# Performance work log

Hardware: AMD Instinct MI355X
Metric: run time of the kernel (lower is better)

The kernel has to match this reference:

```python
import jax, jax.numpy as jnp
import numpy as np

N_NODES = 100000
N_EDGES = 640000
D = 128
L = 3
NUM_GRAPHS = 128


def setup_inputs() -> dict:
    key = jax.random.key(0)
    ks = jax.random.split(key, 8)
    scale = 1.0 / np.sqrt(D)
    x = jax.random.normal(ks[0], (N_NODES, D), dtype=jnp.float32)
    edge_index = jax.random.randint(ks[1], (2, N_EDGES), 0, N_NODES, dtype=jnp.int64)
    batch = jnp.sort(jax.random.randint(ks[2], (N_NODES,), 0, NUM_GRAPHS, dtype=jnp.int64))
    W1 = jax.random.normal(ks[3], (L, D, D), dtype=jnp.float32) * scale
    b1 = jnp.zeros((L, D), dtype=jnp.float32)
    W2 = jax.random.normal(ks[4], (L, D, D), dtype=jnp.float32) * scale
    b2 = jnp.zeros((L, D), dtype=jnp.float32)
    return {"x": x, "edge_index": edge_index, "batch": batch,
            "W1": W1, "b1": b1, "W2": W2, "b2": b2}


def reference(x, edge_index, batch, W1, b1, W2, b2):
    # GIN forward: per layer z = ReLU(MLP((1+eps)*z + sum_{j in N(i)} z_j)), eps=0
    n = x.shape[0]
    src, dst = edge_index[0], edge_index[1]  # messages flow src -> dst
    z = x
    for l in range(W1.shape[0]):
        agg = jax.ops.segment_sum(z[src], dst, num_segments=n)  # scatter-add aggregation
        h = agg + z                                             # (1+eps)*x_i + sum x_j, eps=0
        h = jnp.maximum(h @ W1[l] + b1[l], 0.0)                 # Linear + ReLU
        z = h @ W2[l] + b2[l]                                   # Linear
        z = jnp.maximum(z, 0.0)                                 # F.relu after conv
    # global mean pool over graph ids (dropout is identity in eval / p=0)
    ones = jnp.ones((n,), dtype=z.dtype)
    counts = jax.ops.segment_sum(ones, batch, num_segments=NUM_GRAPHS)
    sums = jax.ops.segment_sum(z, batch, num_segments=NUM_GRAPHS)
    g = sums / jnp.maximum(counts, 1.0)[:, None]
    return z, g
```

## Files before the change

### kernel.cpp

```cpp
#include <hip/hip_runtime.h>
#include <hip/hip_bf16.h>

#define D 128
#define NG 128
#define PROWS 128

typedef __attribute__((ext_vector_type(8))) short bf16x8;
typedef __attribute__((ext_vector_type(4))) float f32x4;

__device__ inline unsigned short f2bf(float f) {
  union { float f; unsigned u; } c; c.f = f;
  unsigned u = c.u;
  return (unsigned short)((u + 0x7FFFu + ((u >> 16) & 1u)) >> 16);
}
__device__ inline float bf2f(unsigned short b) {
  union { unsigned u; float f; } c; c.u = ((unsigned)b) << 16;
  return c.f;
}

__global__ void prep_w(const float* __restrict__ W1, const float* __restrict__ W2,
                       unsigned short* __restrict__ Wt1, unsigned short* __restrict__ Wt2,
                       int* __restrict__ deg, int N) {
  int t = blockIdx.x * 256 + threadIdx.x;
  if (t < N) deg[t] = 0;
  if (t >= 3 * 128 * 128) return;
  int l = t >> 14, k = (t >> 7) & 127, n = t & 127;
  int o = (l << 14) + (n << 7) + k;
  Wt1[o] = f2bf(W1[t]);
  Wt2[o] = f2bf(W2[t]);
}


__global__ void hist_deg(const int* __restrict__ dst, int* __restrict__ deg, int E) {
  int e = blockIdx.x * 256 + threadIdx.x;
  if (e < E) atomicAdd(deg + dst[e], 1);
}

__global__ __launch_bounds__(256) void scan1(const int* __restrict__ deg,
    int* __restrict__ rowptr, int* __restrict__ bsum, int n) {
  __shared__ int sh[256];
  int tid = threadIdx.x;
  int idx = blockIdx.x * 1024 + tid * 4;
  int v[4], tsum = 0;
#pragma unroll
  for (int j = 0; j < 4; ++j) { v[j] = (idx + j < n) ? deg[idx + j] : 0; tsum += v[j]; }
  sh[tid] = tsum;
  __syncthreads();
  for (int off = 1; off < 256; off <<= 1) {
    int x = (tid >= off) ? sh[tid - off] : 0;
    __syncthreads();
    sh[tid] += x;
    __syncthreads();
  }
  if (tid == 255) bsum[blockIdx.x] = sh[255];
  int run = sh[tid] - tsum;
#pragma unroll
  for (int j = 0; j < 4; ++j) { if (idx + j < n) rowptr[idx + j] = run; run += v[j]; }
}

__global__ __launch_bounds__(128) void scan2(int* __restrict__ bsum, int nb) {
  __shared__ int sh[128];
  int tid = threadIdx.x;
  int v = (tid < nb) ? bsum[tid] : 0;
  sh[tid] = v;
  __syncthreads();
  for (int off = 1; off < 128; off <<= 1) {
    int x = (tid >= off) ? sh[tid - off] : 0;
    __syncthreads();
    sh[tid] += x;
    __syncthreads();
  }
  if (tid < nb) bsum[tid] = sh[tid] - v;
}

__global__ void scan3(int* __restrict__ rowptr, int* __restrict__ pos,
                      const int* __restrict__ bsum, int n, int E) {
  int t = blockIdx.x * 256 + threadIdx.x;
  if (t < n) {
    int v = rowptr[t] + bsum[t >> 10];
    rowptr[t] = v;
    pos[t] = v;
  }
  if (t == 0) rowptr[n] = E;
}

__global__ void edge_scatter(const int* __restrict__ src, const int* __restrict__ dst,
                             int* __restrict__ pos, int* __restrict__ csr_src, int E) {
  int e = blockIdx.x * 256 + threadIdx.x;
  if (e >= E) return;
  int idx = atomicAdd(pos + dst[e], 1);
  csr_src[idx] = src[e];
}


template<bool IN_BF16, bool LAST>
__global__ __launch_bounds__(256) void layer_fused(const void* __restrict__ zin,
    const int* __restrict__ rowptr, const int* __restrict__ csr_src,
    const unsigned short* __restrict__ Wt1, const float* __restrict__ b1v,
    const unsigned short* __restrict__ Wt2, const float* __restrict__ b2v,
    unsigned short* __restrict__ Zb, float* __restrict__ Zf, int M) {
  __shared__ unsigned short lds[128][136];
  int tid = threadIdx.x;
  int base = blockIdx.x * 128;
  const float* zf = (const float*)zin;
  const unsigned short* zb = (const unsigned short*)zin;

  int g = tid >> 3;
  int lanei = tid & 7;
  int c = lanei * 16;

#pragma unroll 1
  for (int rr = 0; rr < 4; ++rr) {
    int rl = g * 4 + rr;
    int row = base + rl;
    if (row >= M) row = M - 1;
    float acc[16];

    if constexpr (IN_BF16) {
      const unsigned short* p = zb + (size_t)row * D + c;
      bf16x8 v0 = *(const bf16x8*)(p);
      bf16x8 v1 = *(const bf16x8*)(p + 8);
#pragma unroll
      for (int j = 0; j < 8; ++j) {
        acc[j]     = bf2f((unsigned short)v0[j]);
        acc[j + 8] = bf2f((unsigned short)v1[j]);
      }
    } else {
      const float* p = zf + (size_t)row * D + c;
      float4 v0 = *(const float4*)(p);
      float4 v1 = *(const float4*)(p + 4);
      float4 v2 = *(const float4*)(p + 8);
      float4 v3 = *(const float4*)(p + 12);
      acc[0]  = v0.x; acc[1]  = v0.y; acc[2]  = v0.z; acc[3]  = v0.w;
      acc[4]  = v1.x; acc[5]  = v1.y; acc[6]  = v1.z; acc[7]  = v1.w;
      acc[8]  = v2.x; acc[9]  = v2.y; acc[10] = v2.z; acc[11] = v2.w;
      acc[12] = v3.x; acc[13] = v3.y; acc[14] = v3.z; acc[15] = v3.w;
    }

    int e  = rowptr[row];
    int e1 = rowptr[row + 1];

    if constexpr (IN_BF16) {
      for (; e + 4 <= e1; e += 4) {
        int s0 = csr_src[e + 0];
        int s1 = csr_src[e + 1];
        int s2 = csr_src[e + 2];
        int s3 = csr_src[e + 3];
        const unsigned short* p0 = zb + (size_t)s0 * D + c;
        const unsigned short* p1 = zb + (size_t)s1 * D + c;
        const unsigned short* p2 = zb + (size_t)s2 * D + c;
        const unsigned short* p3 = zb + (size_t)s3 * D + c;
        bf16x8 a0 = *(const bf16x8*)(p0), a1 = *(const bf16x8*)(p0 + 8);
        bf16x8 b0 = *(const bf16x8*)(p1), b1 = *(const bf16x8*)(p1 + 8);
        bf16x8 c0 = *(const bf16x8*)(p2), c1 = *(const bf16x8*)(p2 + 8);
        bf16x8 d0 = *(const bf16x8*)(p3), d1 = *(const bf16x8*)(p3 + 8);
#pragma unroll
        for (int j = 0; j < 8; ++j) {
          acc[j]     += (bf2f((unsigned short)a0[j]) + bf2f((unsigned short)b0[j]))
                      + (bf2f((unsigned short)c0[j]) + bf2f((unsigned short)d0[j]));
          acc[j + 8] += (bf2f((unsigned short)a1[j]) + bf2f((unsigned short)b1[j]))
                      + (bf2f((unsigned short)c1[j]) + bf2f((unsigned short)d1[j]));
        }
      }
      if (e + 2 <= e1) {
        int s0 = csr_src[e + 0];
        int s1 = csr_src[e + 1];
        const unsigned short* p0 = zb + (size_t)s0 * D + c;
        const unsigned short* p1 = zb + (size_t)s1 * D + c;
        bf16x8 a0 = *(const bf16x8*)(p0), a1 = *(const bf16x8*)(p0 + 8);
        bf16x8 b0 = *(const bf16x8*)(p1), b1 = *(const bf16x8*)(p1 + 8);
#pragma unroll
        for (int j = 0; j < 8; ++j) {
          acc[j]     += bf2f((unsigned short)a0[j]) + bf2f((unsigned short)b0[j]);
          acc[j + 8] += bf2f((unsigned short)a1[j]) + bf2f((unsigned short)b1[j]);
        }
        e += 2;
      }
      if (e < e1) {
        int s0 = csr_src[e];
        const unsigned short* p0 = zb + (size_t)s0 * D + c;
        bf16x8 a0 = *(const bf16x8*)(p0), a1 = *(const bf16x8*)(p0 + 8);
#pragma unroll
        for (int j = 0; j < 8; ++j) {
          acc[j]     += bf2f((unsigned short)a0[j]);
          acc[j + 8] += bf2f((unsigned short)a1[j]);
        }
      }
    } else {
      for (; e + 2 <= e1; e += 2) {
        int s0 = csr_src[e + 0];
        int s1 = csr_src[e + 1];
        const float* p0 = zf + (size_t)s0 * D + c;
        const float* p1 = zf + (size_t)s1 * D + c;
        float4 u0 = *(const float4*)(p0);
        float4 u1 = *(const float4*)(p0 + 4);
        float4 u2 = *(const float4*)(p0 + 8);
        float4 u3 = *(const float4*)(p0 + 12);
        float4 w0 = *(const float4*)(p1);
        float4 w1 = *(const float4*)(p1 + 4);
        float4 w2 = *(const float4*)(p1 + 8);
        float4 w3 = *(const float4*)(p1 + 12);
        acc[0]  += u0.x + w0.x; acc[1]  += u0.y + w0.y;
        acc[2]  += u0.z + w0.z; acc[3]  += u0.w + w0.w;
        acc[4]  += u1.x + w1.x; acc[5]  += u1.y + w1.y;
        acc[6]  += u1.z + w1.z; acc[7]  += u1.w + w1.w;
        acc[8]  += u2.x + w2.x; acc[9]  += u2.y + w2.y;
        acc[10] += u2.z + w2.z; acc[11] += u2.w + w2.w;
        acc[12] += u3.x + w3.x; acc[13] += u3.y + w3.y;
        acc[14] += u3.z + w3.z; acc[15] += u3.w + w3.w;
      }
      if (e < e1) {
        int s0 = csr_src[e];
        const float* p0 = zf + (size_t)s0 * D + c;
        float4 u0 = *(const float4*)(p0);
        float4 u1 = *(const float4*)(p0 + 4);
        float4 u2 = *(const float4*)(p0 + 8);
        float4 u3 = *(const float4*)(p0 + 12);
        acc[0]  += u0.x; acc[1]  += u0.y; acc[2]  += u0.z; acc[3]  += u0.w;
        acc[4]  += u1.x; acc[5]  += u1.y; acc[6]  += u1.z; acc[7]  += u1.w;
        acc[8]  += u2.x; acc[9]  += u2.y; acc[10] += u2.z; acc[11] += u2.w;
        acc[12] += u3.x; acc[13] += u3.y; acc[14] += u3.z; acc[15] += u3.w;
      }
    }

    bf16x8 o0, o1;
#pragma unroll
    for (int j = 0; j < 8; ++j) {
      o0[j] = (short)f2bf(acc[j]);
      o1[j] = (short)f2bf(acc[j + 8]);
    }
    *(bf16x8*)&lds[rl][c]     = o0;
    *(bf16x8*)&lds[rl][c + 8] = o1;
  }
  __syncthreads();

  int lane = tid & 63;
  int wid  = tid >> 6;
  int row_base = base + wid * 32;
  int c16 = lane & 15;
  int kq  = lane >> 4;
  int koff = kq * 8;

  bf16x8 a[2][4];
#pragma unroll
  for (int fr = 0; fr < 2; ++fr)
#pragma unroll
    for (int kk = 0; kk < 4; ++kk)
      a[fr][kk] = *(const bf16x8*)&lds[wid * 32 + fr * 16 + c16][kk * 32 + koff];
  __syncthreads();

#pragma unroll
  for (int fc = 0; fc < 8; ++fc) {
    f32x4 acc0 = {0.f, 0.f, 0.f, 0.f};
    f32x4 acc1 = {0.f, 0.f, 0.f, 0.f};
    int col = fc * 16 + c16;
#pragma unroll
    for (int kk = 0; kk < 4; ++kk) {
      bf16x8 b = *(const bf16x8*)(Wt1 + (size_t)col * D + kk * 32 + koff);
      acc0 = __builtin_amdgcn_mfma_f32_16x16x32_bf16(a[0][kk], b, acc0, 0, 0, 0);
      acc1 = __builtin_amdgcn_mfma_f32_16x16x32_bf16(a[1][kk], b, acc1, 0, 0, 0);
    }
    float bv = b1v[col];
#pragma unroll
    for (int r = 0; r < 4; ++r) {
      int rl = kq * 4 + r;
      lds[wid * 32 + rl][col]      = f2bf(fmaxf(acc0[r] + bv, 0.f));
      lds[wid * 32 + rl + 16][col] = f2bf(fmaxf(acc1[r] + bv, 0.f));
    }
  }
  __syncthreads();

  bf16x8 a2[2][4];
#pragma unroll
  for (int fr = 0; fr < 2; ++fr)
#pragma unroll
    for (int kk = 0; kk < 4; ++kk)
      a2[fr][kk] = *(const bf16x8*)&lds[wid * 32 + fr * 16 + c16][kk * 32 + koff];

#pragma unroll
  for (int fc = 0; fc < 8; ++fc) {
    f32x4 acc0 = {0.f, 0.f, 0.f, 0.f};
    f32x4 acc1 = {0.f, 0.f, 0.f, 0.f};
    int col = fc * 16 + c16;
#pragma unroll
    for (int kk = 0; kk < 4; ++kk) {
      bf16x8 b = *(const bf16x8*)(Wt2 + (size_t)col * D + kk * 32 + koff);
      acc0 = __builtin_amdgcn_mfma_f32_16x16x32_bf16(a2[0][kk], b, acc0, 0, 0, 0);
      acc1 = __builtin_amdgcn_mfma_f32_16x16x32_bf16(a2[1][kk], b, acc1, 0, 0, 0);
    }
    float bv = b2v[col];
#pragma unroll
    for (int r = 0; r < 4; ++r) {
      int row0 = row_base + kq * 4 + r;
      float v0 = fmaxf(acc0[r] + bv, 0.f);
      if (row0 < M) {
        if constexpr (LAST) Zf[(size_t)row0 * D + col] = v0;
        else                Zb[(size_t)row0 * D + col] = f2bf(v0);
      }
      int row1 = row0 + 16;
      float v1 = fmaxf(acc1[r] + bv, 0.f);
      if (row1 < M) {
        if constexpr (LAST) Zf[(size_t)row1 * D + col] = v1;
        else                Zb[(size_t)row1 * D + col] = f2bf(v1);
      }
    }
  }
}


__global__ void pool_zero(float* __restrict__ g, int* __restrict__ counts) {
  int t = blockIdx.x * 256 + threadIdx.x;
  if (t < NG * D) g[t] = 0.f;
  if (t < NG) counts[t] = 0;
}

__global__ __launch_bounds__(128) void pool_accum(const float* __restrict__ z,
    const int* __restrict__ batch, float* __restrict__ g, int* __restrict__ counts, int N) {
  int col = threadIdx.x;
  int r0 = blockIdx.x * PROWS;
  if (r0 >= N) return;
  int r1 = min(r0 + PROWS, N);
  float acc = 0.f;
  int cur = batch[r0];
  int segstart = r0;
  for (int i = r0; i < r1; ++i) {
    int b = batch[i];
    if (b != cur) {
      atomicAdd(g + (size_t)cur * D + col, acc);
      if (col == 0) atomicAdd(counts + cur, i - segstart);
      acc = 0.f; cur = b; segstart = i;
    }
    acc += z[(size_t)i * D + col];
  }
  atomicAdd(g + (size_t)cur * D + col, acc);
  if (col == 0) atomicAdd(counts + cur, r1 - segstart);
}

__global__ void pool_div(float* __restrict__ g, const int* __restrict__ counts) {
  int t = blockIdx.x * 256 + threadIdx.x;
  if (t >= NG * D) return;
  g[t] = g[t] / fmaxf((float)counts[t >> 7], 1.f);
}

extern "C" void kernel_launch(void* const* d_in, const int* in_sizes, int n_in,
                              void* d_out, int out_size, void* d_ws, size_t ws_size,
                              hipStream_t stream) {
  const float* x     = (const float*)d_in[0];
  const int*   ei    = (const int*)d_in[1];
  const int*   batch = (const int*)d_in[2];
  const float* W1    = (const float*)d_in[3];
  const float* b1    = (const float*)d_in[4];
  const float* W2    = (const float*)d_in[5];
  const float* b2    = (const float*)d_in[6];

  const int N = in_sizes[0] / D;
  const int E = in_sizes[1] / 2;
  const int* src = ei;
  const int* dst = ei + E;

  float* zout = (float*)d_out;
  float* g    = zout + (size_t)N * D;

  char* w = (char*)d_ws;
  unsigned short* zb_a    = (unsigned short*)w;    w += (size_t)N * D * 2;
  unsigned short* zb_b    = (unsigned short*)w;    w += (size_t)N * D * 2;
  unsigned short* Wt1     = (unsigned short*)w;    w += 3 * 16384 * 2;
  unsigned short* Wt2     = (unsigned short*)w;    w += 3 * 16384 * 2;
  int*            counts  = (int*)w;               w += NG * 4;
  int*            deg     = (int*)w;               w += (size_t)N * 4;
  int*            rowptr  = (int*)w;               w += (size_t)(N + 4) * 4;
  int*            pos     = (int*)w;               w += (size_t)N * 4;
  int*            bsum    = (int*)w;               w += 128 * 4;
  int*            csr_src = (int*)w;               w += (size_t)E * 4;

  const int nb = (N + 1023) / 1024;

  int prep_threads = (3 * 128 * 128 > N) ? 3 * 128 * 128 : N;
  prep_w<<<(prep_threads + 255) / 256, 256, 0, stream>>>(W1, W2, Wt1, Wt2, deg, N);

  hist_deg<<<(E + 255) / 256, 256, 0, stream>>>(dst, deg, E);
  scan1<<<nb, 256, 0, stream>>>(deg, rowptr, bsum, N);
  scan2<<<1, 128, 0, stream>>>(bsum, nb);
  scan3<<<(N + 255) / 256, 256, 0, stream>>>(rowptr, pos, bsum, N, E);
  edge_scatter<<<(E + 255) / 256, 256, 0, stream>>>(src, dst, pos, csr_src, E);

  const int blocks = (N + 127) / 128;

  layer_fused<false, false><<<blocks, 256, 0, stream>>>(x, rowptr, csr_src,
      Wt1, b1, Wt2, b2, zb_a, zout, N);
  layer_fused<true, false><<<blocks, 256, 0, stream>>>(zb_a, rowptr, csr_src,
      Wt1 + 16384, b1 + 128, Wt2 + 16384, b2 + 128, zb_b, zout, N);
  layer_fused<true, true><<<blocks, 256, 0, stream>>>(zb_b, rowptr, csr_src,
      Wt1 + 32768, b1 + 256, Wt2 + 32768, b2 + 256, zb_a, zout, N);

  pool_zero<<<(NG * D + 255) / 256, 256, 0, stream>>>(g, counts);
  pool_accum<<<(N + PROWS - 1) / PROWS, 128, 0, stream>>>(zout, batch, g, counts, N);
  pool_div<<<(NG * D + 255) / 256, 256, 0, stream>>>(g, counts);
}
```

Before: 338.2 us.

## Split fused layer into separate gather-aggregate and MLP GEMM kernels

Each layer's single fused kernel becomes two: a gather kernel with one node per 8 threads that writes the bf16 aggregate to a workspace, and a GEMM kernel over 64-row tiles that runs both linears with MFMA and writes coalesced bf16 output through LDS. Zeroing of the pool buffers moves into the prep kernel, removing one launch. The aim is more parallelism and better latency hiding for the irregular gather, away from the serial 4-row loop per thread group and the LDS-bound large block. The cost is an extra bf16 round trip of the aggregate through global memory plus more launches per layer.

```diff
diff --git a/kernel.cpp b/kernel.cpp
--- a/kernel.cpp
+++ b/kernel.cpp
@@ -20,9 +20,12 @@
 
 __global__ void prep_w(const float* __restrict__ W1, const float* __restrict__ W2,
                        unsigned short* __restrict__ Wt1, unsigned short* __restrict__ Wt2,
-                       int* __restrict__ deg, int N) {
+                       int* __restrict__ deg, int N,
+                       float* __restrict__ g, int* __restrict__ counts) {
   int t = blockIdx.x * 256 + threadIdx.x;
   if (t < N) deg[t] = 0;
+  if (t < NG * D) g[t] = 0.f;
+  if (t < NG) counts[t] = 0;
   if (t >= 3 * 128 * 128) return;
   int l = t >> 14, k = (t >> 7) & 127, n = t & 127;
   int o = (l << 14) + (n << 7) + k;
@@ -93,226 +96,219 @@
 }
 
 
-template<bool IN_BF16, bool LAST>
-__global__ __launch_bounds__(256) void layer_fused(const void* __restrict__ zin,
+template<bool IN_BF16>
+__global__ __launch_bounds__(256) void gather_agg(const void* __restrict__ zin,
     const int* __restrict__ rowptr, const int* __restrict__ csr_src,
+    unsigned short* __restrict__ agg, int N) {
+  int t = blockIdx.x * 256 + threadIdx.x;
+  int node = t >> 3;
+  if (node >= N) return;
+  int c = (t & 7) * 16;
+  const float* zf = (const float*)zin;
+  const unsigned short* zb = (const unsigned short*)zin;
+
+  float acc[16];
+
+  if constexpr (IN_BF16) {
+    const unsigned short* p = zb + (size_t)node * D + c;
+    bf16x8 v0 = *(const bf16x8*)(p);
+    bf16x8 v1 = *(const bf16x8*)(p + 8);
+#pragma unroll
+    for (int j = 0; j < 8; ++j) {
+      acc[j]     = bf2f((unsigned short)v0[j]);
+      acc[j + 8] = bf2f((unsigned short)v1[j]);
+    }
+  } else {
+    const float* p = zf + (size_t)node * D + c;
+    float4 v0 = *(const float4*)(p);
+    float4 v1 = *(const float4*)(p + 4);
+    float4 v2 = *(const float4*)(p + 8);
+    float4 v3 = *(const float4*)(p + 12);
+    acc[0]  = v0.x; acc[1]  = v0.y; acc[2]  = v0.z; acc[3]  = v0.w;
+    acc[4]  = v1.x; acc[5]  = v1.y; acc[6]  = v1.z; acc[7]  = v1.w;
+    acc[8]  = v2.x; acc[9]  = v2.y; acc[10] = v2.z; acc[11] = v2.w;
+    acc[12] = v3.x; acc[13] = v3.y; acc[14] = v3.z; acc[15] = v3.w;
+  }
+
+  int e  = rowptr[node];
+  int e1 = rowptr[node + 1];
+
+  if constexpr (IN_BF16) {
+    for (; e + 4 <= e1; e += 4) {
+      int s0 = csr_src[e + 0];
+      int s1 = csr_src[e + 1];
+      int s2 = csr_src[e + 2];
+      int s3 = csr_src[e + 3];
+      const unsigned short* p0 = zb + (size_t)s0 * D + c;
+      const unsigned short* p1 = zb + (size_t)s1 * D + c;
+      const unsigned short* p2 = zb + (size_t)s2 * D + c;
+      const unsigned short* p3 = zb + (size_t)s3 * D + c;
+      bf16x8 a0 = *(const bf16x8*)(p0), a1 = *(const bf16x8*)(p0 + 8);
+      bf16x8 b0 = *(const bf16x8*)(p1), b1 = *(const bf16x8*)(p1 + 8);
+      bf16x8 c0 = *(const bf16x8*)(p2), c1 = *(const bf16x8*)(p2 + 8);
+      bf16x8 d0 = *(const bf16x8*)(p3), d1 = *(const bf16x8*)(p3 + 8);
+#pragma unroll
+      for (int j = 0; j < 8; ++j) {
+        acc[j]     += (bf2f((unsigned short)a0[j]) + bf2f((unsigned short)b0[j]))
+                    + (bf2f((unsigned short)c0[j]) + bf2f((unsigned short)d0[j]));
+        acc[j + 8] += (bf2f((unsigned short)a1[j]) + bf2f((unsigned short)b1[j]))
+                    + (bf2f((unsigned short)c1[j]) + bf2f((unsigned short)d1[j]));
+      }
+    }
+    if (e + 2 <= e1) {
+      int s0 = csr_src[e + 0];
+      int s1 = csr_src[e + 1];
+      const unsigned short* p0 = zb + (size_t)s0 * D + c;
+      const unsigned short* p1 = zb + (size_t)s1 * D + c;
+      bf16x8 a0 = *(const bf16x8*)(p0), a1 = *(const bf16x8*)(p0 + 8);
+      bf16x8 b0 = *(const bf16x8*)(p1), b1 = *(const bf16x8*)(p1 + 8);
+#pragma unroll
+      for (int j = 0; j < 8; ++j) {
+        acc[j]     += bf2f((unsigned short)a0[j]) + bf2f((unsigned short)b0[j]);
+        acc[j + 8] += bf2f((unsigned short)a1[j]) + bf2f((unsigned short)b1[j]);
+      }
+      e += 2;
+    }
+    if (e < e1) {
+      int s0 = csr_src[e];
+      const unsigned short* p0 = zb + (size_t)s0 * D + c;
+      bf16x8 a0 = *(const bf16x8*)(p0), a1 = *(const bf16x8*)(p0 + 8);
+#pragma unroll
+      for (int j = 0; j < 8; ++j) {
+        acc[j]     += bf2f((unsigned short)a0[j]);
+        acc[j + 8] += bf2f((unsigned short)a1[j]);
+      }
+    }
+  } else {
+    for (; e + 2 <= e1; e += 2) {
+      int s0 = csr_src[e + 0];
+      int s1 = csr_src[e + 1];
+      const float* p0 = zf + (size_t)s0 * D + c;
+      const float* p1 = zf + (size_t)s1 * D + c;
+      float4 u0 = *(const float4*)(p0);
+      float4 u1 = *(const float4*)(p0 + 4);
+      float4 u2 = *(const float4*)(p0 + 8);
+      float4 u3 = *(const float4*)(p0 + 12);
+      float4 w0 = *(const float4*)(p1);
+      float4 w1 = *(const float4*)(p1 + 4);
+      float4 w2 = *(const float4*)(p1 + 8);
+      float4 w3 = *(const float4*)(p1 + 12);
+      acc[0]  += u0.x + w0.x; acc[1]  += u0.y + w0.y;
+      acc[2]  += u0.z + w0.z; acc[3]  += u0.w + w0.w;
+      acc[4]  += u1.x + w1.x; acc[5]  += u1.y + w1.y;
+      acc[6]  += u1.z + w1.z; acc[7]  += u1.w + w1.w;
+      acc[8]  += u2.x + w2.x; acc[9]  += u2.y + w2.y;
+      acc[10] += u2.z + w2.z; acc[11] += u2.w + w2.w;
+      acc[12] += u3.x + w3.x; acc[13] += u3.y + w3.y;
+      acc[14] += u3.z + w3.z; acc[15] += u3.w + w3.w;
+    }
+    if (e < e1) {
+      int s0 = csr_src[e];
+      const float* p0 = zf + (size_t)s0 * D + c;
+      float4 u0 = *(const float4*)(p0);
+      float4 u1 = *(const float4*)(p0 + 4);
+      float4 u2 = *(const float4*)(p0 + 8);
+      float4 u3 = *(const float4*)(p0 + 12);
+      acc[0]  += u0.x; acc[1]  += u0.y; acc[2]  += u0.z; acc[3]  += u0.w;
+      acc[4]  += u1.x; acc[5]  += u1.y; acc[6]  += u1.z; acc[7]  += u1.w;
+      acc[8]  += u2.x; acc[9]  += u2.y; acc[10] += u2.z; acc[11] += u2.w;
+      acc[12] += u3.x; acc[13] += u3.y; acc[14] += u3.z; acc[15] += u3.w;
+    }
+  }
+
+  bf16x8 o0, o1;
+#pragma unroll
+  for (int j = 0; j < 8; ++j) {
+    o0[j] = (short)f2bf(acc[j]);
+    o1[j] = (short)f2bf(acc[j + 8]);
+  }
+  unsigned short* q = agg + (size_t)node * D + c;
+  *(bf16x8*)(q)     = o0;
+  *(bf16x8*)(q + 8) = o1;
+}
+
+
+template<bool LAST>
+__global__ __launch_bounds__(256) void gemm_fused(const unsigned short* __restrict__ A,
     const unsigned short* __restrict__ Wt1, const float* __restrict__ b1v,
     const unsigned short* __restrict__ Wt2, const float* __restrict__ b2v,
     unsigned short* __restrict__ Zb, float* __restrict__ Zf, int M) {
-  __shared__ unsigned short lds[128][136];
-  int tid = threadIdx.x;
-  int base = blockIdx.x * 128;
-  const float* zf = (const float*)zin;
-  const unsigned short* zb = (const unsigned short*)zin;
-
-  int g = tid >> 3;
-  int lanei = tid & 7;
-  int c = lanei * 16;
-
-#pragma unroll 1
-  for (int rr = 0; rr < 4; ++rr) {
-    int rl = g * 4 + rr;
-    int row = base + rl;
-    if (row >= M) row = M - 1;
-    float acc[16];
-
-    if constexpr (IN_BF16) {
-      const unsigned short* p = zb + (size_t)row * D + c;
-      bf16x8 v0 = *(const bf16x8*)(p);
-      bf16x8 v1 = *(const bf16x8*)(p + 8);
-#pragma unroll
-      for (int j = 0; j < 8; ++j) {
-        acc[j]     = bf2f((unsigned short)v0[j]);
-        acc[j + 8] = bf2f((unsigned short)v1[j]);
-      }
-    } else {
-      const float* p = zf + (size_t)row * D + c;
-      float4 v0 = *(const float4*)(p);
-      float4 v1 = *(const float4*)(p + 4);
-      float4 v2 = *(const float4*)(p + 8);
-      float4 v3 = *(const float4*)(p + 12);
-      acc[0]  = v0.x; acc[1]  = v0.y; acc[2]  = v0.z; acc[3]  = v0.w;
-      acc[4]  = v1.x; acc[5]  = v1.y; acc[6]  = v1.z; acc[7]  = v1.w;
-      acc[8]  = v2.x; acc[9]  = v2.y; acc[10] = v2.z; acc[11] = v2.w;
-      acc[12] = v3.x; acc[13] = v3.y; acc[14] = v3.z; acc[15] = v3.w;
-    }
-
-    int e  = rowptr[row];
-    int e1 = rowptr[row + 1];
-
-    if constexpr (IN_BF16) {
-      for (; e + 4 <= e1; e += 4) {
-        int s0 = csr_src[e + 0];
-        int s1 = csr_src[e + 1];
-        int s2 = csr_src[e + 2];
-        int s3 = csr_src[e + 3];
-        const unsigned short* p0 = zb + (size_t)s0 * D + c;
-        const unsigned short* p1 = zb + (size_t)s1 * D + c;
-        const unsigned short* p2 = zb + (size_t)s2 * D + c;
-        const unsigned short* p3 = zb + (size_t)s3 * D + c;
-        bf16x8 a0 = *(const bf16x8*)(p0), a1 = *(const bf16x8*)(p0 + 8);
-        bf16x8 b0 = *(const bf16x8*)(p1), b1 = *(const bf16x8*)(p1 + 8);
-        bf16x8 c0 = *(const bf16x8*)(p2), c1 = *(const bf16x8*)(p2 + 8);
-        bf16x8 d0 = *(const bf16x8*)(p3), d1 = *(const bf16x8*)(p3 + 8);
-#pragma unroll
-        for (int j = 0; j < 8; ++j) {
-          acc[j]     += (bf2f((unsigned short)a0[j]) + bf2f((unsigned short)b0[j]))
-                      + (bf2f((unsigned short)c0[j]) + bf2f((unsigned short)d0[j]));
-          acc[j + 8] += (bf2f((unsigned short)a1[j]) + bf2f((unsigned short)b1[j]))
-                      + (bf2f((unsigned short)c1[j]) + bf2f((unsigned short)d1[j]));
-        }
-      }
-      if (e + 2 <= e1) {
-        int s0 = csr_src[e + 0];
-        int s1 = csr_src[e + 1];
-        const unsigned short* p0 = zb + (size_t)s0 * D + c;
-        const unsigned short* p1 = zb + (size_t)s1 * D + c;
-        bf16x8 a0 = *(const bf16x8*)(p0), a1 = *(const bf16x8*)(p0 + 8);
-        bf16x8 b0 = *(const bf16x8*)(p1), b1 = *(const bf16x8*)(p1 + 8);
-#pragma unroll
-        for (int j = 0; j < 8; ++j) {
-          acc[j]     += bf2f((unsigned short)a0[j]) + bf2f((unsigned short)b0[j]);
-          acc[j + 8] += bf2f((unsigned short)a1[j]) + bf2f((unsigned short)b1[j]);
-        }
-        e += 2;
-      }
-      if (e < e1) {
-        int s0 = csr_src[e];
-        const unsigned short* p0 = zb + (size_t)s0 * D + c;
-        bf16x8 a0 = *(const bf16x8*)(p0), a1 = *(const bf16x8*)(p0 + 8);
-#pragma unroll
-        for (int j = 0; j < 8; ++j) {
-          acc[j]     += bf2f((unsigned short)a0[j]);
-          acc[j + 8] += bf2f((unsigned short)a1[j]);
-        }
-      }
-    } else {
-      for (; e + 2 <= e1; e += 2) {
-        int s0 = csr_src[e + 0];
-        int s1 = csr_src[e + 1];
-        const float* p0 = zf + (size_t)s0 * D + c;
-        const float* p1 = zf + (size_t)s1 * D + c;
-        float4 u0 = *(const float4*)(p0);
-        float4 u1 = *(const float4*)(p0 + 4);
-        float4 u2 = *(const float4*)(p0 + 8);
-        float4 u3 = *(const float4*)(p0 + 12);
-        float4 w0 = *(const float4*)(p1);
-        float4 w1 = *(const float4*)(p1 + 4);
-        float4 w2 = *(const float4*)(p1 + 8);
-        float4 w3 = *(const float4*)(p1 + 12);
-        acc[0]  += u0.x + w0.x; acc[1]  += u0.y + w0.y;
-        acc[2]  += u0.z + w0.z; acc[3]  += u0.w + w0.w;
-        acc[4]  += u1.x + w1.x; acc[5]  += u1.y + w1.y;
-        acc[6]  += u1.z + w1.z; acc[7]  += u1.w + w1.w;
-        acc[8]  += u2.x + w2.x; acc[9]  += u2.y + w2.y;
-        acc[10] += u2.z + w2.z; acc[11] += u2.w + w2.w;
-        acc[12] += u3.x + w3.x; acc[13] += u3.y + w3.y;
-        acc[14] += u3.z + w3.z; acc[15] += u3.w + w3.w;
-      }
-      if (e < e1) {
-        int s0 = csr_src[e];
-        const float* p0 = zf + (size_t)s0 * D + c;
-        float4 u0 = *(const float4*)(p0);
-        float4 u1 = *(const float4*)(p0 + 4);
-        float4 u2 = *(const float4*)(p0 + 8);
-        float4 u3 = *(const float4*)(p0 + 12);
-        acc[0]  += u0.x; acc[1]  += u0.y; acc[2]  += u0.z; acc[3]  += u0.w;
-        acc[4]  += u1.x; acc[5]  += u1.y; acc[6]  += u1.z; acc[7]  += u1.w;
-        acc[8]  += u2.x; acc[9]  += u2.y; acc[10] += u2.z; acc[11] += u2.w;
-        acc[12] += u3.x; acc[13] += u3.y; acc[14] += u3.z; acc[15] += u3.w;
-      }
-    }
-
-    bf16x8 o0, o1;
-#pragma unroll
-    for (int j = 0; j < 8; ++j) {
-      o0[j] = (short)f2bf(acc[j]);
-      o1[j] = (short)f2bf(acc[j + 8]);
-    }
-    *(bf16x8*)&lds[rl][c]     = o0;
-    *(bf16x8*)&lds[rl][c + 8] = o1;
-  }
-  __syncthreads();
-
-  int lane = tid & 63;
-  int wid  = tid >> 6;
-  int row_base = base + wid * 32;
+  __shared__ unsigned short hs[4][16][136];
+  int lane = threadIdx.x & 63;
+  int wid  = threadIdx.x >> 6;
+  int rb = blockIdx.x * 64 + wid * 16;
   int c16 = lane & 15;
   int kq  = lane >> 4;
   int koff = kq * 8;
 
-  bf16x8 a[2][4];
-#pragma unroll
-  for (int fr = 0; fr < 2; ++fr)
-#pragma unroll
-    for (int kk = 0; kk < 4; ++kk)
-      a[fr][kk] = *(const bf16x8*)&lds[wid * 32 + fr * 16 + c16][kk * 32 + koff];
-  __syncthreads();
+  bf16x8 a[4];
+  {
+    int row = rb + c16;
+    if (row >= M) row = M - 1;
+    const unsigned short* p = A + (size_t)row * D + koff;
+#pragma unroll
+    for (int kk = 0; kk < 4; ++kk) a[kk] = *(const bf16x8*)(p + kk * 32);
+  }
 
 #pragma unroll
   for (int fc = 0; fc < 8; ++fc) {
-    f32x4 acc0 = {0.f, 0.f, 0.f, 0.f};
-    f32x4 acc1 = {0.f, 0.f, 0.f, 0.f};
+    f32x4 acc = {0.f, 0.f, 0.f, 0.f};
     int col = fc * 16 + c16;
 #pragma unroll
     for (int kk = 0; kk < 4; ++kk) {
       bf16x8 b = *(const bf16x8*)(Wt1 + (size_t)col * D + kk * 32 + koff);
-      acc0 = __builtin_amdgcn_mfma_f32_16x16x32_bf16(a[0][kk], b, acc0, 0, 0, 0);
-      acc1 = __builtin_amdgcn_mfma_f32_16x16x32_bf16(a[1][kk], b, acc1, 0, 0, 0);
+      acc = __builtin_amdgcn_mfma_f32_16x16x32_bf16(a[kk], b, acc, 0, 0, 0);
     }
     float bv = b1v[col];
 #pragma unroll
-    for (int r = 0; r < 4; ++r) {
-      int rl = kq * 4 + r;
-      lds[wid * 32 + rl][col]      = f2bf(fmaxf(acc0[r] + bv, 0.f));
-      lds[wid * 32 + rl + 16][col] = f2bf(fmaxf(acc1[r] + bv, 0.f));
-    }
+    for (int r = 0; r < 4; ++r)
+      hs[wid][kq * 4 + r][col] = f2bf(fmaxf(acc[r] + bv, 0.f));
   }
   __syncthreads();
 
-  bf16x8 a2[2][4];
-#pragma unroll
-  for (int fr = 0; fr < 2; ++fr)
-#pragma unroll
-    for (int kk = 0; kk < 4; ++kk)
-      a2[fr][kk] = *(const bf16x8*)&lds[wid * 32 + fr * 16 + c16][kk * 32 + koff];
+  bf16x8 a2[4];
+#pragma unroll
+  for (int kk = 0; kk < 4; ++kk)
+    a2[kk] = *(const bf16x8*)&hs[wid][c16][kk * 32 + koff];
+  if constexpr (!LAST) __syncthreads();
 
 #pragma unroll
   for (int fc = 0; fc < 8; ++fc) {
-    f32x4 acc0 = {0.f, 0.f, 0.f, 0.f};
-    f32x4 acc1 = {0.f, 0.f, 0.f, 0.f};
+    f32x4 acc = {0.f, 0.f, 0.f, 0.f};
     int col = fc * 16 + c16;
 #pragma unroll
     for (int kk = 0; kk < 4; ++kk) {
       bf16x8 b = *(const bf16x8*)(Wt2 + (size_t)col * D + kk * 32 + koff);
-      acc0 = __builtin_amdgcn_mfma_f32_16x16x32_bf16(a2[0][kk], b, acc0, 0, 0, 0);
-      acc1 = __builtin_amdgcn_mfma_f32_16x16x32_bf16(a2[1][kk], b, acc1, 0, 0, 0);
+      acc = __builtin_amdgcn_mfma_f32_16x16x32_bf16(a2[kk], b, acc, 0, 0, 0);
     }
     float bv = b2v[col];
-#pragma unroll
-    for (int r = 0; r < 4; ++r) {
-      int row0 = row_base + kq * 4 + r;
-      float v0 = fmaxf(acc0[r] + bv, 0.f);
-      if (row0 < M) {
-        if constexpr (LAST) Zf[(size_t)row0 * D + col] = v0;
-        else                Zb[(size_t)row0 * D + col] = f2bf(v0);
+    if constexpr (LAST) {
+#pragma unroll
+      for (int r = 0; r < 4; ++r) {
+        int row = rb + kq * 4 + r;
+        if (row < M) Zf[(size_t)row * D + col] = fmaxf(acc[r] + bv, 0.f);
       }
-      int row1 = row0 + 16;
-      float v1 = fmaxf(acc1[r] + bv, 0.f);
-      if (row1 < M) {
-        if constexpr (LAST) Zf[(size_t)row1 * D + col] = v1;
-        else                Zb[(size_t)row1 * D + col] = f2bf(v1);
-      }
-    }
-  }
-}
-
-
-__global__ void pool_zero(float* __restrict__ g, int* __restrict__ counts) {
-  int t = blockIdx.x * 256 + threadIdx.x;
-  if (t < NG * D) g[t] = 0.f;
-  if (t < NG) counts[t] = 0;
-}
+    } else {
+#pragma unroll
+      for (int r = 0; r < 4; ++r)
+        hs[wid][kq * 4 + r][col] = f2bf(fmaxf(acc[r] + bv, 0.f));
+    }
+  }
+
+  if constexpr (!LAST) {
+    __syncthreads();
+#pragma unroll
+    for (int i = 0; i < 4; ++i) {
+      int rl = i * 4 + kq;
+      int ce = c16 * 8;
+      bf16x8 v = *(const bf16x8*)&hs[wid][rl][ce];
+      int row = rb + rl;
+      if (row < M)
+        *(bf16x8*)(Zb + (size_t)row * D + ce) = v;
+    }
+  }
+}
+
 
 __global__ __launch_bounds__(128) void pool_accum(const float* __restrict__ z,
     const int* __restrict__ batch, float* __restrict__ g, int* __restrict__ counts, int N) {
@@ -362,8 +358,8 @@
   float* g    = zout + (size_t)N * D;
 
   char* w = (char*)d_ws;
-  unsigned short* zb_a    = (unsigned short*)w;    w += (size_t)N * D * 2;
-  unsigned short* zb_b    = (unsigned short*)w;    w += (size_t)N * D * 2;
+  unsigned short* agg     = (unsigned short*)w;    w += (size_t)N * D * 2;
+  unsigned short* zb      = (unsigned short*)w;    w += (size_t)N * D * 2;
   unsigned short* Wt1     = (unsigned short*)w;    w += 3 * 16384 * 2;
   unsigned short* Wt2     = (unsigned short*)w;    w += 3 * 16384 * 2;
   int*            counts  = (int*)w;               w += NG * 4;
@@ -376,7 +372,7 @@
   const int nb = (N + 1023) / 1024;
 
   int prep_threads = (3 * 128 * 128 > N) ? 3 * 128 * 128 : N;
-  prep_w<<<(prep_threads + 255) / 256, 256, 0, stream>>>(W1, W2, Wt1, Wt2, deg, N);
+  prep_w<<<(prep_threads + 255) / 256, 256, 0, stream>>>(W1, W2, Wt1, Wt2, deg, N, g, counts);
 
   hist_deg<<<(E + 255) / 256, 256, 0, stream>>>(dst, deg, E);
   scan1<<<nb, 256, 0, stream>>>(deg, rowptr, bsum, N);
@@ -384,16 +380,18 @@
   scan3<<<(N + 255) / 256, 256, 0, stream>>>(rowptr, pos, bsum, N, E);
   edge_scatter<<<(E + 255) / 256, 256, 0, stream>>>(src, dst, pos, csr_src, E);
 
-  const int blocks = (N + 127) / 128;
-
-  layer_fused<false, false><<<blocks, 256, 0, stream>>>(x, rowptr, csr_src,
-      Wt1, b1, Wt2, b2, zb_a, zout, N);
-  layer_fused<true, false><<<blocks, 256, 0, stream>>>(zb_a, rowptr, csr_src,
-      Wt1 + 16384, b1 + 128, Wt2 + 16384, b2 + 128, zb_b, zout, N);
-  layer_fused<true, true><<<blocks, 256, 0, stream>>>(zb_b, rowptr, csr_src,
-      Wt1 + 32768, b1 + 256, Wt2 + 32768, b2 + 256, zb_a, zout, N);
-
-  pool_zero<<<(NG * D + 255) / 256, 256, 0, stream>>>(g, counts);
+  const int gather_blocks = (int)(((size_t)N * 8 + 255) / 256);
+  const int gemm_blocks   = (N + 63) / 64;
+
+  gather_agg<false><<<gather_blocks, 256, 0, stream>>>(x, rowptr, csr_src, agg, N);
+  gemm_fused<false><<<gemm_blocks, 256, 0, stream>>>(agg, Wt1, b1, Wt2, b2, zb, zout, N);
+  gather_agg<true><<<gather_blocks, 256, 0, stream>>>(zb, rowptr, csr_src, agg, N);
+  gemm_fused<false><<<gemm_blocks, 256, 0, stream>>>(agg, Wt1 + 16384, b1 + 128,
+                                                     Wt2 + 16384, b2 + 128, zb, zout, N);
+  gather_agg<true><<<gather_blocks, 256, 0, stream>>>(zb, rowptr, csr_src, agg, N);
+  gemm_fused<true><<<gemm_blocks, 256, 0, stream>>>(agg, Wt1 + 32768, b1 + 256,
+                                                    Wt2 + 32768, b2 + 256, zb, zout, N);
+
   pool_accum<<<(N + PROWS - 1) / PROWS, 128, 0, stream>>>(zout, batch, g, counts, N);
   pool_div<<<(NG * D + 255) / 256, 256, 0, stream>>>(g, counts);
 }
```

Result: slower. 413.3 us (+22.2%).
